# Optimization experiments

Measured on AMD Instinct MI355X. Metric: run time of the kernel, lower is better.

Reference implementation:

```python
import jax, jax.numpy as jnp
import numpy as np

B, L, D, H = 4, 2048, 1024, 16
DH = D // H
EPS = 1e-6

def layer_norm(x, g, b):
    mu = jnp.mean(x, axis=-1, keepdims=True)
    var = jnp.mean(jnp.square(x - mu), axis=-1, keepdims=True)
    return (x - mu) * jax.lax.rsqrt(var + EPS) * g + b

def setup_inputs() -> dict:
    key = jax.random.key(0)
    ks = jax.random.split(key, 8)
    s = 0.02
    return {
        "x": jax.random.normal(ks[0], (B, L, D), jnp.float32),
        "mask": jnp.ones((B, L), jnp.int32),
        "Wq": jax.random.normal(ks[1], (D, D), jnp.float32) * s,
        "bq": jnp.zeros((D,), jnp.float32),
        "Wk": jax.random.normal(ks[2], (D, D), jnp.float32) * s,
        "bk": jnp.zeros((D,), jnp.float32),
        "Wv": jax.random.normal(ks[3], (D, D), jnp.float32) * s,
        "bv": jnp.zeros((D,), jnp.float32),
        "g1": jnp.ones((D,), jnp.float32),
        "b1": jnp.zeros((D,), jnp.float32),
        "g2": jnp.ones((D,), jnp.float32),
        "b2": jnp.zeros((D,), jnp.float32),
        "Wo1": jax.random.normal(ks[4], (D, D), jnp.float32) * s,
        "bo1": jnp.zeros((D,), jnp.float32),
        "Wo2": jax.random.normal(ks[5], (D, D), jnp.float32) * s,
        "bo2": jnp.zeros((D,), jnp.float32),
    }

def reference(x, mask, Wq, bq, Wk, bk, Wv, bv, g1, b1, g2, b2, Wo1, bo1, Wo2, bo2):
    h = layer_norm(x, g1, b1)                                  # [B,L,D]
    q = (h @ Wq + bq).reshape(B, L, H, DH)
    k = (h @ Wk + bk).reshape(B, L, H, DH)
    v = (h @ Wv + bv).reshape(B, L, H, DH)
    scores = jnp.einsum('bqhd,bkhd->bhqk', q, k) / jnp.sqrt(jnp.float32(DH))
    m = mask.astype(scores.dtype)[:, None, None, :]            # [B,1,1,L]
    scores = scores + (1.0 - m) * (-1e30)                      # mask_logits
    probs = jax.nn.softmax(scores, axis=-1)
    attn = jnp.einsum('bhqk,bkhd->bqhd', probs, v).reshape(B, L, D)
    residual = x + attn
    out = layer_norm(residual, g2, b2)
    out = jax.nn.gelu(out @ Wo1 + bo1, approximate=False)      # exact GELU (nn.GELU)
    out = out @ Wo2 + bo2 + residual
    return out
```

## Files before the change

### kernel.cpp

```cpp
#include <hip/hip_runtime.h>
#include <stdint.h>
#include <math.h>

typedef __bf16 bf16_t;
typedef __bf16 bf16x8 __attribute__((ext_vector_type(8)));
typedef __bf16 bf16x4 __attribute__((ext_vector_type(4)));
typedef short short4v __attribute__((ext_vector_type(4)));
typedef float f32x4 __attribute__((ext_vector_type(4)));

#define B_ 4
#define L_ 2048
#define D_ 1024
#define H_ 16
#define DH_ 64
#define M_ (B_ * L_)
#define LOG2E 1.4426950408889634f
#define QSCALE 0.18033688011112042f

__device__ __forceinline__ void gload16(const bf16_t* gsrc, bf16_t* ldst) {
    __builtin_amdgcn_global_load_lds(
        (__attribute__((address_space(1))) void*)(void*)(gsrc),
        (__attribute__((address_space(3))) void*)(ldst), 16, 0, 0);
}

__device__ __forceinline__ float gelu_exact(float v) {
    return 0.5f * v * (1.0f + erff(v * 0.70710678118654752f));
}

__device__ __forceinline__ float fast_exp2(float x) {
#if __has_builtin(__builtin_amdgcn_exp2f)
    return __builtin_amdgcn_exp2f(x);
#else
    return exp2f(x);
#endif
}

__device__ __forceinline__ f32x4 mfma16(bf16x4 a, bf16x4 b, f32x4 c) {
#if __has_builtin(__builtin_amdgcn_mfma_f32_16x16x16_bf16)
    return __builtin_amdgcn_mfma_f32_16x16x16_bf16(a, b, c, 0, 0, 0);
#else
    union U { bf16x4 h; short4v s; };
    U ua, ub; ua.h = a; ub.h = b;
    return __builtin_amdgcn_mfma_f32_16x16x16bf16_1k(ua.s, ub.s, c, 0, 0, 0);
#endif
}

__global__ __launch_bounds__(256) void transpose5(const float* __restrict__ W0, const float* __restrict__ W1,
                                                  const float* __restrict__ W2, const float* __restrict__ W3,
                                                  const float* __restrict__ W4,
                                                  bf16_t* __restrict__ T0, bf16_t* __restrict__ T1,
                                                  bf16_t* __restrict__ T2, bf16_t* __restrict__ T3,
                                                  bf16_t* __restrict__ T4) {
    const float* W; bf16_t* T;
    switch (blockIdx.z) {
        case 0: W = W0; T = T0; break;
        case 1: W = W1; T = T1; break;
        case 2: W = W2; T = T2; break;
        case 3: W = W3; T = T3; break;
        default: W = W4; T = T4; break;
    }
    __shared__ float tile[32][33];
    const int x = threadIdx.x, y0 = threadIdx.y;
    const int bx = blockIdx.x * 32, by = blockIdx.y * 32;
    for (int kk = 0; kk < 4; ++kk)
        tile[y0 + kk * 8][x] = W[(size_t)(by + y0 + kk * 8) * D_ + bx + x];
    __syncthreads();
    for (int kk = 0; kk < 4; ++kk)
        T[(size_t)(bx + y0 + kk * 8) * D_ + by + x] = (bf16_t)tile[x][y0 + kk * 8];
}

__global__ __launch_bounds__(256) void maskbias_kernel(const int* __restrict__ mask,
                                                       float* __restrict__ mb) {
    const int i = blockIdx.x * 256 + threadIdx.x;
    mb[i] = mask[i] ? 0.f : -1.0e30f;
}

#define VTR_STRIDE 76
__global__ __launch_bounds__(256) void vtrans_kernel(const bf16_t* __restrict__ vb,
                                                     bf16_t* __restrict__ vt) {
    __shared__ bf16_t tile[128 * VTR_STRIDE];
    const int t = threadIdx.x;
    const int bh = blockIdx.y, b = bh >> 4, h = bh & 15;
    const int k0 = blockIdx.x * 128;
    #pragma unroll
    for (int it = 0; it < 4; ++it) {
        const int row = it * 32 + (t >> 3), c8 = (t & 7) * 8;
        *(uint4*)&tile[row * VTR_STRIDE + c8] =
            *(const uint4*)(vb + (size_t)(b * L_ + k0 + row) * D_ + h * DH_ + c8);
    }
    __syncthreads();
    #pragma unroll
    for (int it = 0; it < 4; ++it) {
        const int d = it * 16 + (t >> 4), kg = (t & 15) * 8;
        union { uint4 u; bf16_t e[8]; } tv;
        #pragma unroll
        for (int j = 0; j < 8; ++j) tv.e[j] = tile[(kg + j) * VTR_STRIDE + d];
        *(uint4*)&vt[((size_t)bh * DH_ + d) * L_ + k0 + kg] = tv.u;
    }
}

__global__ __launch_bounds__(256) void ln1_kernel(const float* __restrict__ x,
                                                  const float* __restrict__ g,
                                                  const float* __restrict__ b,
                                                  bf16_t* __restrict__ h) {
    const int row = blockIdx.x, t = threadIdx.x;
    const float4 v = *(const float4*)(x + (size_t)row * D_ + t * 4);
    float s = v.x + v.y + v.z + v.w;
    float s2 = v.x * v.x + v.y * v.y + v.z * v.z + v.w * v.w;
    for (int m = 1; m < 64; m <<= 1) { s += __shfl_xor(s, m, 64); s2 += __shfl_xor(s2, m, 64); }
    __shared__ float red[2][4];
    if ((t & 63) == 0) { red[0][t >> 6] = s; red[1][t >> 6] = s2; }
    __syncthreads();
    s = red[0][0] + red[0][1] + red[0][2] + red[0][3];
    s2 = red[1][0] + red[1][1] + red[1][2] + red[1][3];
    const float mean = s * (1.f / 1024.f);
    const float var = s2 * (1.f / 1024.f) - mean * mean;
    const float rstd = rsqrtf(var + 1e-6f);
    const float4 gv = *(const float4*)(g + t * 4);
    const float4 bv = *(const float4*)(b + t * 4);
    union { bf16_t h4[4]; uint2 u; } o;
    o.h4[0] = (bf16_t)((v.x - mean) * rstd * gv.x + bv.x);
    o.h4[1] = (bf16_t)((v.y - mean) * rstd * gv.y + bv.y);
    o.h4[2] = (bf16_t)((v.z - mean) * rstd * gv.z + bv.z);
    o.h4[3] = (bf16_t)((v.w - mean) * rstd * gv.w + bv.w);
    *(uint2*)(h + (size_t)row * D_ + t * 4) = o.u;
}

__global__ __launch_bounds__(256) void add_ln2_kernel(const float* __restrict__ x,
                                                      const bf16_t* __restrict__ attnb,
                                                      const float* __restrict__ g,
                                                      const float* __restrict__ b,
                                                      bf16_t* __restrict__ residb,
                                                      bf16_t* __restrict__ h) {
    const int row = blockIdx.x, t = threadIdx.x;
    const float4 xv = *(const float4*)(x + (size_t)row * D_ + t * 4);
    union { uint2 u; bf16_t h4[4]; } ai;
    ai.u = *(const uint2*)(attnb + (size_t)row * D_ + t * 4);
    float4 v;
    v.x = xv.x + (float)ai.h4[0]; v.y = xv.y + (float)ai.h4[1];
    v.z = xv.z + (float)ai.h4[2]; v.w = xv.w + (float)ai.h4[3];
    union { bf16_t h4[4]; uint2 u; } rs;
    rs.h4[0] = (bf16_t)v.x; rs.h4[1] = (bf16_t)v.y; rs.h4[2] = (bf16_t)v.z; rs.h4[3] = (bf16_t)v.w;
    *(uint2*)(residb + (size_t)row * D_ + t * 4) = rs.u;
    float s = v.x + v.y + v.z + v.w;
    float s2 = v.x * v.x + v.y * v.y + v.z * v.z + v.w * v.w;
    for (int m = 1; m < 64; m <<= 1) { s += __shfl_xor(s, m, 64); s2 += __shfl_xor(s2, m, 64); }
    __shared__ float red[2][4];
    if ((t & 63) == 0) { red[0][t >> 6] = s; red[1][t >> 6] = s2; }
    __syncthreads();
    s = red[0][0] + red[0][1] + red[0][2] + red[0][3];
    s2 = red[1][0] + red[1][1] + red[1][2] + red[1][3];
    const float mean = s * (1.f / 1024.f);
    const float var = s2 * (1.f / 1024.f) - mean * mean;
    const float rstd = rsqrtf(var + 1e-6f);
    const float4 gv = *(const float4*)(g + t * 4);
    const float4 bv = *(const float4*)(b + t * 4);
    union { bf16_t h4[4]; uint2 u; } o;
    o.h4[0] = (bf16_t)((v.x - mean) * rstd * gv.x + bv.x);
    o.h4[1] = (bf16_t)((v.y - mean) * rstd * gv.y + bv.y);
    o.h4[2] = (bf16_t)((v.z - mean) * rstd * gv.z + bv.z);
    o.h4[3] = (bf16_t)((v.w - mean) * rstd * gv.w + bv.w);
    *(uint2*)(h + (size_t)row * D_ + t * 4) = o.u;
}

__global__ __launch_bounds__(256) void gemm_qkv(const bf16_t* __restrict__ A,
                                                const bf16_t* __restrict__ BT,
                                                const float* __restrict__ bq,
                                                const float* __restrict__ bk,
                                                const float* __restrict__ bv,
                                                bf16_t* __restrict__ qb,
                                                bf16_t* __restrict__ kb,
                                                bf16_t* __restrict__ vb) {
    constexpr int K = 1024;
    __shared__ bf16_t As[128 * 32];
    __shared__ bf16_t Bs[128 * 32];
    const int t = threadIdx.x;
    const int wave = t >> 6, lane = t & 63;
    const int l16 = lane & 15, g4 = lane >> 4;
    const int bm = blockIdx.x * 128, bn = blockIdx.y * 128;
    const int wm = (wave >> 1) * 64, wn = (wave & 1) * 64;

    f32x4 acc[4][4];
    for (int i = 0; i < 4; ++i)
        for (int j = 0; j < 4; ++j) acc[i][j] = (f32x4){0.f, 0.f, 0.f, 0.f};

    const int ar = t >> 2, ak = (t & 3) * 8;
    const bf16_t* Ag = A + (size_t)(bm + ar) * K + ak;
    const bf16_t* Bg = BT + (size_t)(bn + ar) * K + ak;
    bf16_t* Al = As + t * 8;
    bf16_t* Bl = Bs + t * 8;

    for (int kk = 0; kk < K; kk += 32) {
        __syncthreads();
        gload16(Ag + kk, Al);
        gload16(Ag + (size_t)64 * K + kk, Al + 2048);
        gload16(Bg + kk, Bl);
        gload16(Bg + (size_t)64 * K + kk, Bl + 2048);
        __syncthreads();
        bf16x8 af[4], bfr[4];
        for (int i = 0; i < 4; ++i)
            af[i] = *(const bf16x8*)&As[(wm + i * 16 + l16) * 32 + g4 * 8];
        for (int j = 0; j < 4; ++j)
            bfr[j] = *(const bf16x8*)&Bs[(wn + j * 16 + l16) * 32 + g4 * 8];
        for (int i = 0; i < 4; ++i)
            for (int j = 0; j < 4; ++j)
                acc[i][j] = __builtin_amdgcn_mfma_f32_16x16x32_bf16(af[i], bfr[j], acc[i][j], 0, 0, 0);
    }

    const int which = bn >> 10;
    const int c0 = bn & 1023;
    const float* bias = (which == 0) ? bq : (which == 1) ? bk : bv;
    bf16_t* ob = (which == 0) ? qb : (which == 1) ? kb : vb;
    const float scale = (which == 0) ? QSCALE : 1.0f;

    for (int i = 0; i < 4; ++i)
        for (int j = 0; j < 4; ++j) {
            const int col = c0 + wn + j * 16 + l16;
            const float bvv = bias[col];
            const int row0 = bm + wm + i * 16 + g4 * 4;
            for (int r = 0; r < 4; ++r) {
                const float vv = (acc[i][j][r] + bvv) * scale;
                ob[(size_t)(row0 + r) * D_ + col] = (bf16_t)vv;
            }
        }
}

template <int MODE>
__global__ __launch_bounds__(256) void gemm_bt(const bf16_t* __restrict__ A,
                                               const bf16_t* __restrict__ BT,
                                               const float* __restrict__ bias,
                                               const bf16_t* __restrict__ residb,
                                               bf16_t* __restrict__ outb,
                                               float* __restrict__ outf) {
    constexpr int K = 1024, N = 1024;
    __shared__ bf16_t As[128 * 32];
    __shared__ bf16_t Bs[128 * 32];
    const int t = threadIdx.x;
    const int wave = t >> 6, lane = t & 63;
    const int l16 = lane & 15, g4 = lane >> 4;
    const int bm = blockIdx.x * 128, bn = blockIdx.y * 128;
    const int wm = (wave >> 1) * 64, wn = (wave & 1) * 64;

    f32x4 acc[4][4];
    for (int i = 0; i < 4; ++i)
        for (int j = 0; j < 4; ++j) acc[i][j] = (f32x4){0.f, 0.f, 0.f, 0.f};

    const int ar = t >> 2, ak = (t & 3) * 8;
    const bf16_t* Ag = A + (size_t)(bm + ar) * K + ak;
    const bf16_t* Bg = BT + (size_t)(bn + ar) * K + ak;
    bf16_t* Al = As + t * 8;
    bf16_t* Bl = Bs + t * 8;

    for (int kk = 0; kk < K; kk += 32) {
        __syncthreads();
        gload16(Ag + kk, Al);
        gload16(Ag + (size_t)64 * K + kk, Al + 2048);
        gload16(Bg + kk, Bl);
        gload16(Bg + (size_t)64 * K + kk, Bl + 2048);
        __syncthreads();
        bf16x8 af[4], bfr[4];
        for (int i = 0; i < 4; ++i)
            af[i] = *(const bf16x8*)&As[(wm + i * 16 + l16) * 32 + g4 * 8];
        for (int j = 0; j < 4; ++j)
            bfr[j] = *(const bf16x8*)&Bs[(wn + j * 16 + l16) * 32 + g4 * 8];
        for (int i = 0; i < 4; ++i)
            for (int j = 0; j < 4; ++j)
                acc[i][j] = __builtin_amdgcn_mfma_f32_16x16x32_bf16(af[i], bfr[j], acc[i][j], 0, 0, 0);
    }

    for (int i = 0; i < 4; ++i)
        for (int j = 0; j < 4; ++j) {
            const int col = bn + wn + j * 16 + l16;
            const float bv = bias[col];
            const int row0 = bm + wm + i * 16 + g4 * 4;
            for (int r = 0; r < 4; ++r) {
                float vv = acc[i][j][r] + bv;
                const size_t idx = (size_t)(row0 + r) * N + col;
                if (MODE == 1) {
                    outb[idx] = (bf16_t)gelu_exact(vv);
                } else {
                    outf[idx] = vv + (float)residb[idx];
                }
            }
        }
}

#define VT_STRIDE 152
#define OS_STRIDE 72
__global__ __launch_bounds__(256, 3) void attn_kernel(const bf16_t* __restrict__ q,
                                                      const bf16_t* __restrict__ k,
                                                      const bf16_t* __restrict__ vt,
                                                      const float* __restrict__ maskbias,
                                                      bf16_t* __restrict__ attnb) {
    __shared__ bf16_t Ks[128 * 64];
    __shared__ bf16_t VT[64 * VT_STRIDE];
    bf16_t* Os = VT;

    const int t = threadIdx.x;
    const int wave = t >> 6, lane = t & 63;
    const int l16 = lane & 15, g4 = lane >> 4;
    const int id = blockIdx.x;
    const int xcd = id & 7, seq = id >> 3;
    const int bh = xcd * 8 + (seq >> 4);
    const int b = bh >> 4, h = bh & 15;
    const int q0 = (seq & 15) * 128;

    bf16x8 qf[2][2];
    for (int ti = 0; ti < 2; ++ti)
        for (int c = 0; c < 2; ++c)
            qf[ti][c] = *(const bf16x8*)(q + (size_t)(b * L_ + q0 + wave * 32 + ti * 16 + l16) * D_ +
                                         h * DH_ + c * 32 + g4 * 8);

    f32x4 accO[2][5];
    for (int ti = 0; ti < 2; ++ti)
        for (int dt = 0; dt < 5; ++dt) accO[ti][dt] = (f32x4){0.f, 0.f, 0.f, 0.f};

    const bf16_t one_or_zero = (l16 == 0) ? (bf16_t)1.0f : (bf16_t)0.0f;
    const bf16x4 ones4 = (bf16x4){one_or_zero, one_or_zero, one_or_zero, one_or_zero};

    const int krow0 = t >> 3, kcg = t & 7;
    const int klcg = kcg ^ (krow0 & 7);
    const bf16_t* kbase = k + (size_t)(b * L_ + krow0) * D_ + h * DH_ + klcg * 8;
    bf16_t* kdst = Ks + t * 8;
    const int vrow0 = t >> 4, vkg = t & 15;
    const bf16_t* vbase = vt + ((size_t)bh * DH_ + vrow0) * L_ + vkg * 8;
    bf16_t* vdst = &VT[vrow0 * VT_STRIDE + vkg * 8];

    const int kb0 = l16 * 64 + ((g4 ^ (l16 & 7)) * 8);
    const int kb1 = l16 * 64 + (((g4 + 4) ^ (l16 & 7)) * 8);
    const int vrb = l16 * VT_STRIDE + g4 * 4;

    for (int k0 = 0; k0 < L_; k0 += 128) {
        __syncthreads();
        #pragma unroll
        for (int it = 0; it < 4; ++it)
            gload16(kbase + (size_t)(k0 + it * 32) * D_, kdst + it * 2048);
        #pragma unroll
        for (int it = 0; it < 4; ++it) {
            const uint4 vv = *(const uint4*)(vbase + (size_t)(it * 16) * L_ + k0);
            *(uint4*)(vdst + it * 16 * VT_STRIDE) = vv;
        }
        __syncthreads();

        f32x4 s0[8], s1[8];
        #pragma unroll
        for (int tj = 0; tj < 8; ++tj) {
            const bf16x8 kf0 = *(const bf16x8*)&Ks[tj * 1024 + kb0];
            const bf16x8 kf1 = *(const bf16x8*)&Ks[tj * 1024 + kb1];
            f32x4 a = (f32x4){0.f, 0.f, 0.f, 0.f};
            a = __builtin_amdgcn_mfma_f32_16x16x32_bf16(kf0, qf[0][0], a, 0, 0, 0);
            a = __builtin_amdgcn_mfma_f32_16x16x32_bf16(kf1, qf[0][1], a, 0, 0, 0);
            s0[tj] = a;
            f32x4 a2 = (f32x4){0.f, 0.f, 0.f, 0.f};
            a2 = __builtin_amdgcn_mfma_f32_16x16x32_bf16(kf0, qf[1][0], a2, 0, 0, 0);
            a2 = __builtin_amdgcn_mfma_f32_16x16x32_bf16(kf1, qf[1][1], a2, 0, 0, 0);
            s1[tj] = a2;
        }

        bf16x4 pb0[8], pb1[8];
        #pragma unroll
        for (int tj = 0; tj < 8; ++tj) {
            const float4 mb = *(const float4*)&maskbias[b * L_ + k0 + tj * 16 + g4 * 4];
            float p00 = fast_exp2(s0[tj][0] + mb.x), p01 = fast_exp2(s0[tj][1] + mb.y);
            float p02 = fast_exp2(s0[tj][2] + mb.z), p03 = fast_exp2(s0[tj][3] + mb.w);
            float p10 = fast_exp2(s1[tj][0] + mb.x), p11 = fast_exp2(s1[tj][1] + mb.y);
            float p12 = fast_exp2(s1[tj][2] + mb.z), p13 = fast_exp2(s1[tj][3] + mb.w);
            pb0[tj] = (bf16x4){(bf16_t)p00, (bf16_t)p01, (bf16_t)p02, (bf16_t)p03};
            pb1[tj] = (bf16x4){(bf16_t)p10, (bf16_t)p11, (bf16_t)p12, (bf16_t)p13};
        }

        #pragma unroll
        for (int ks = 0; ks < 8; ++ks) {
            #pragma unroll
            for (int dt = 0; dt < 4; ++dt) {
                const bf16x4 va = *(const bf16x4*)&VT[vrb + dt * 16 * VT_STRIDE + ks * 16];
                accO[0][dt] = mfma16(va, pb0[ks], accO[0][dt]);
                accO[1][dt] = mfma16(va, pb1[ks], accO[1][dt]);
            }
            accO[0][4] = mfma16(ones4, pb0[ks], accO[0][4]);
            accO[1][4] = mfma16(ones4, pb1[ks], accO[1][4]);
        }
    }

    __syncthreads();
    for (int ti = 0; ti < 2; ++ti) {
        const float lv = __shfl(accO[ti][4][0], l16, 64);
        const float rl = 1.0f / lv;
        #pragma unroll
        for (int dt = 0; dt < 4; ++dt) {
            bf16x4 o4 = (bf16x4){(bf16_t)(accO[ti][dt][0] * rl), (bf16_t)(accO[ti][dt][1] * rl),
                                 (bf16_t)(accO[ti][dt][2] * rl), (bf16_t)(accO[ti][dt][3] * rl)};
            *(bf16x4*)&Os[(wave * 32 + ti * 16 + l16) * OS_STRIDE + dt * 16 + g4 * 4] = o4;
        }
    }
    __syncthreads();
    for (int cc = 0; cc < 4; ++cc) {
        const int c2 = t + cc * 256;
        const int row = c2 >> 3, k8 = c2 & 7;
        const uint4 vv = *(const uint4*)&Os[row * OS_STRIDE + k8 * 8];
        *(uint4*)&attnb[(size_t)(b * L_ + q0 + row) * D_ + h * DH_ + k8 * 8] = vv;
    }
}

extern "C" void kernel_launch(void* const* d_in, const int* in_sizes, int n_in,
                              void* d_out, int out_size, void* d_ws, size_t ws_size,
                              hipStream_t stream) {
    const float* x    = (const float*)d_in[0];
    const int*   mask = (const int*)d_in[1];
    const float* Wq   = (const float*)d_in[2];
    const float* bq   = (const float*)d_in[3];
    const float* Wk   = (const float*)d_in[4];
    const float* bk   = (const float*)d_in[5];
    const float* Wv   = (const float*)d_in[6];
    const float* bv   = (const float*)d_in[7];
    const float* g1   = (const float*)d_in[8];
    const float* b1   = (const float*)d_in[9];
    const float* g2   = (const float*)d_in[10];
    const float* b2   = (const float*)d_in[11];
    const float* Wo1  = (const float*)d_in[12];
    const float* bo1  = (const float*)d_in[13];
    const float* Wo2  = (const float*)d_in[14];
    const float* bo2  = (const float*)d_in[15];

    char* ws = (char*)d_ws;
    const size_t MBs = 1ull << 20;
    bf16_t* WqkvT = (bf16_t*)(ws + 0 * MBs);
    bf16_t* Wo1T  = (bf16_t*)(ws + 6 * MBs);
    bf16_t* Wo2T  = (bf16_t*)(ws + 8 * MBs);
    bf16_t* h1    = (bf16_t*)(ws + 10 * MBs);
    bf16_t* vtb   = h1;
    bf16_t* qb    = (bf16_t*)(ws + 26 * MBs);
    bf16_t* kb    = (bf16_t*)(ws + 42 * MBs);
    bf16_t* vb    = (bf16_t*)(ws + 58 * MBs);
    bf16_t* attnb = (bf16_t*)(ws + 74 * MBs);
    bf16_t* residb= (bf16_t*)(ws + 90 * MBs);
    float*  mbias = (float*)(ws + 106 * MBs);
    bf16_t* h2    = qb;
    bf16_t* gact  = kb;

    transpose5<<<dim3(32, 32, 5), dim3(32, 8), 0, stream>>>(
        Wq, Wk, Wv, Wo1, Wo2,
        WqkvT, WqkvT + (size_t)D_ * D_, WqkvT + (size_t)2 * D_ * D_, Wo1T, Wo2T);

    maskbias_kernel<<<M_ / 256, 256, 0, stream>>>(mask, mbias);

    ln1_kernel<<<M_, 256, 0, stream>>>(x, g1, b1, h1);

    gemm_qkv<<<dim3(M_ / 128, 3 * D_ / 128), 256, 0, stream>>>(h1, WqkvT, bq, bk, bv, qb, kb, vb);

    vtrans_kernel<<<dim3(L_ / 128, B_ * H_), 256, 0, stream>>>(vb, vtb);

    attn_kernel<<<dim3(1024), 256, 0, stream>>>(qb, kb, vtb, mbias, attnb);

    add_ln2_kernel<<<M_, 256, 0, stream>>>(x, attnb, g2, b2, residb, h2);

    const dim3 gg(M_ / 128, D_ / 128);
    gemm_bt<1><<<gg, 256, 0, stream>>>(h2, Wo1T, bo1, nullptr, gact, nullptr);
    gemm_bt<2><<<gg, 256, 0, stream>>>(gact, Wo2T, bo2, residb, nullptr, (float*)d_out);
}
```

Measured before the change: 374.9 us.

## Skip mask-bias loads for fully-unmasked key tiles and use 16x16x32 MFMA for PV

```diff
diff --git a/kernel.cpp b/kernel.cpp
--- a/kernel.cpp
+++ b/kernel.cpp
@@ -5,7 +5,6 @@
 typedef __bf16 bf16_t;
 typedef __bf16 bf16x8 __attribute__((ext_vector_type(8)));
 typedef __bf16 bf16x4 __attribute__((ext_vector_type(4)));
-typedef short short4v __attribute__((ext_vector_type(4)));
 typedef float f32x4 __attribute__((ext_vector_type(4)));
 
 #define B_ 4
@@ -14,7 +13,6 @@
 #define H_ 16
 #define DH_ 64
 #define M_ (B_ * L_)
-#define LOG2E 1.4426950408889634f
 #define QSCALE 0.18033688011112042f
 
 __device__ __forceinline__ void gload16(const bf16_t* gsrc, bf16_t* ldst) {
@@ -32,16 +30,6 @@
     return __builtin_amdgcn_exp2f(x);
 #else
     return exp2f(x);
-#endif
-}
-
-__device__ __forceinline__ f32x4 mfma16(bf16x4 a, bf16x4 b, f32x4 c) {
-#if __has_builtin(__builtin_amdgcn_mfma_f32_16x16x16_bf16)
-    return __builtin_amdgcn_mfma_f32_16x16x16_bf16(a, b, c, 0, 0, 0);
-#else
-    union U { bf16x4 h; short4v s; };
-    U ua, ub; ua.h = a; ub.h = b;
-    return __builtin_amdgcn_mfma_f32_16x16x16bf16_1k(ua.s, ub.s, c, 0, 0, 0);
 #endif
 }
 
@@ -70,9 +58,18 @@
 }
 
 __global__ __launch_bounds__(256) void maskbias_kernel(const int* __restrict__ mask,
-                                                       float* __restrict__ mb) {
+                                                       float* __restrict__ mb,
+                                                       unsigned char* __restrict__ flags) {
     const int i = blockIdx.x * 256 + threadIdx.x;
-    mb[i] = mask[i] ? 0.f : -1.0e30f;
+    const int m = mask[i];
+    mb[i] = m ? 0.f : -1.0e30f;
+    const unsigned long long bal = __ballot(m != 0);
+    __shared__ unsigned char ok[4];
+    if ((threadIdx.x & 63) == 0) ok[threadIdx.x >> 6] = (bal == ~0ull) ? 1 : 0;
+    __syncthreads();
+    if (threadIdx.x < 2)
+        flags[blockIdx.x * 2 + threadIdx.x] =
+            (unsigned char)(ok[threadIdx.x * 2] & ok[threadIdx.x * 2 + 1]);
 }
 
 #define VTR_STRIDE 76
@@ -91,11 +88,15 @@
     __syncthreads();
     #pragma unroll
     for (int it = 0; it < 4; ++it) {
-        const int d = it * 16 + (t >> 4), kg = (t & 15) * 8;
+        const int d = it * 16 + (t >> 4), pos0 = (t & 15) * 8;
+        const int base32 = pos0 & ~31, g = (pos0 >> 3) & 3;
         union { uint4 u; bf16_t e[8]; } tv;
         #pragma unroll
-        for (int j = 0; j < 8; ++j) tv.e[j] = tile[(kg + j) * VTR_STRIDE + d];
-        *(uint4*)&vt[((size_t)bh * DH_ + d) * L_ + k0 + kg] = tv.u;
+        for (int j = 0; j < 8; ++j) {
+            const int kk = base32 + ((j >> 2) << 4) + (g << 2) + (j & 3);
+            tv.e[j] = tile[kk * VTR_STRIDE + d];
+        }
+        *(uint4*)&vt[((size_t)bh * DH_ + d) * L_ + k0 + pos0] = tv.u;
     }
 }
 
@@ -291,6 +292,7 @@
                                                       const bf16_t* __restrict__ k,
                                                       const bf16_t* __restrict__ vt,
                                                       const float* __restrict__ maskbias,
+                                                      const unsigned char* __restrict__ mflags,
                                                       bf16_t* __restrict__ attnb) {
     __shared__ bf16_t Ks[128 * 64];
     __shared__ bf16_t VT[64 * VT_STRIDE];
@@ -315,8 +317,8 @@
     for (int ti = 0; ti < 2; ++ti)
         for (int dt = 0; dt < 5; ++dt) accO[ti][dt] = (f32x4){0.f, 0.f, 0.f, 0.f};
 
-    const bf16_t one_or_zero = (l16 == 0) ? (bf16_t)1.0f : (bf16_t)0.0f;
-    const bf16x4 ones4 = (bf16x4){one_or_zero, one_or_zero, one_or_zero, one_or_zero};
+    const bf16_t ozv = (l16 == 0) ? (bf16_t)1.0f : (bf16_t)0.0f;
+    const bf16x8 ones8 = (bf16x8){ozv, ozv, ozv, ozv, ozv, ozv, ozv, ozv};
 
     const int krow0 = t >> 3, kcg = t & 7;
     const int klcg = kcg ^ (krow0 & 7);
@@ -328,7 +330,8 @@
 
     const int kb0 = l16 * 64 + ((g4 ^ (l16 & 7)) * 8);
     const int kb1 = l16 * 64 + (((g4 + 4) ^ (l16 & 7)) * 8);
-    const int vrb = l16 * VT_STRIDE + g4 * 4;
+    const int vrb = l16 * VT_STRIDE + g4 * 8;
+    const unsigned char* flg = mflags + b * 16;
 
     for (int k0 = 0; k0 < L_; k0 += 128) {
         __syncthreads();
@@ -357,28 +360,38 @@
             s1[tj] = a2;
         }
 
-        bf16x4 pb0[8], pb1[8];
-        #pragma unroll
-        for (int tj = 0; tj < 8; ++tj) {
-            const float4 mb = *(const float4*)&maskbias[b * L_ + k0 + tj * 16 + g4 * 4];
-            float p00 = fast_exp2(s0[tj][0] + mb.x), p01 = fast_exp2(s0[tj][1] + mb.y);
-            float p02 = fast_exp2(s0[tj][2] + mb.z), p03 = fast_exp2(s0[tj][3] + mb.w);
-            float p10 = fast_exp2(s1[tj][0] + mb.x), p11 = fast_exp2(s1[tj][1] + mb.y);
-            float p12 = fast_exp2(s1[tj][2] + mb.z), p13 = fast_exp2(s1[tj][3] + mb.w);
-            pb0[tj] = (bf16x4){(bf16_t)p00, (bf16_t)p01, (bf16_t)p02, (bf16_t)p03};
-            pb1[tj] = (bf16x4){(bf16_t)p10, (bf16_t)p11, (bf16_t)p12, (bf16_t)p13};
-        }
-
-        #pragma unroll
-        for (int ks = 0; ks < 8; ++ks) {
+        if (!flg[k0 >> 7]) {
+            #pragma unroll
+            for (int tj = 0; tj < 8; ++tj) {
+                const float4 mb = *(const float4*)&maskbias[b * L_ + k0 + tj * 16 + g4 * 4];
+                s0[tj][0] += mb.x; s0[tj][1] += mb.y; s0[tj][2] += mb.z; s0[tj][3] += mb.w;
+                s1[tj][0] += mb.x; s1[tj][1] += mb.y; s1[tj][2] += mb.z; s1[tj][3] += mb.w;
+            }
+        }
+
+        bf16x8 pb0[4], pb1[4];
+        #pragma unroll
+        for (int c = 0; c < 4; ++c) {
+            pb0[c] = (bf16x8){(bf16_t)fast_exp2(s0[2 * c][0]), (bf16_t)fast_exp2(s0[2 * c][1]),
+                              (bf16_t)fast_exp2(s0[2 * c][2]), (bf16_t)fast_exp2(s0[2 * c][3]),
+                              (bf16_t)fast_exp2(s0[2 * c + 1][0]), (bf16_t)fast_exp2(s0[2 * c + 1][1]),
+                              (bf16_t)fast_exp2(s0[2 * c + 1][2]), (bf16_t)fast_exp2(s0[2 * c + 1][3])};
+            pb1[c] = (bf16x8){(bf16_t)fast_exp2(s1[2 * c][0]), (bf16_t)fast_exp2(s1[2 * c][1]),
+                              (bf16_t)fast_exp2(s1[2 * c][2]), (bf16_t)fast_exp2(s1[2 * c][3]),
+                              (bf16_t)fast_exp2(s1[2 * c + 1][0]), (bf16_t)fast_exp2(s1[2 * c + 1][1]),
+                              (bf16_t)fast_exp2(s1[2 * c + 1][2]), (bf16_t)fast_exp2(s1[2 * c + 1][3])};
+        }
+
+        #pragma unroll
+        for (int c = 0; c < 4; ++c) {
             #pragma unroll
             for (int dt = 0; dt < 4; ++dt) {
-                const bf16x4 va = *(const bf16x4*)&VT[vrb + dt * 16 * VT_STRIDE + ks * 16];
-                accO[0][dt] = mfma16(va, pb0[ks], accO[0][dt]);
-                accO[1][dt] = mfma16(va, pb1[ks], accO[1][dt]);
+                const bf16x8 va = *(const bf16x8*)&VT[vrb + dt * 16 * VT_STRIDE + c * 32];
+                accO[0][dt] = __builtin_amdgcn_mfma_f32_16x16x32_bf16(va, pb0[c], accO[0][dt], 0, 0, 0);
+                accO[1][dt] = __builtin_amdgcn_mfma_f32_16x16x32_bf16(va, pb1[c], accO[1][dt], 0, 0, 0);
             }
-            accO[0][4] = mfma16(ones4, pb0[ks], accO[0][4]);
-            accO[1][4] = mfma16(ones4, pb1[ks], accO[1][4]);
+            accO[0][4] = __builtin_amdgcn_mfma_f32_16x16x32_bf16(ones8, pb0[c], accO[0][4], 0, 0, 0);
+            accO[1][4] = __builtin_amdgcn_mfma_f32_16x16x32_bf16(ones8, pb1[c], accO[1][4], 0, 0, 0);
         }
     }
 
@@ -435,6 +448,7 @@
     bf16_t* attnb = (bf16_t*)(ws + 74 * MBs);
     bf16_t* residb= (bf16_t*)(ws + 90 * MBs);
     float*  mbias = (float*)(ws + 106 * MBs);
+    unsigned char* mflags = (unsigned char*)(ws + 107 * MBs);
     bf16_t* h2    = qb;
     bf16_t* gact  = kb;
 
@@ -442,7 +456,7 @@
         Wq, Wk, Wv, Wo1, Wo2,
         WqkvT, WqkvT + (size_t)D_ * D_, WqkvT + (size_t)2 * D_ * D_, Wo1T, Wo2T);
 
-    maskbias_kernel<<<M_ / 256, 256, 0, stream>>>(mask, mbias);
+    maskbias_kernel<<<M_ / 256, 256, 0, stream>>>(mask, mbias, mflags);
 
     ln1_kernel<<<M_, 256, 0, stream>>>(x, g1, b1, h1);
 
@@ -450,7 +464,7 @@
 
     vtrans_kernel<<<dim3(L_ / 128, B_ * H_), 256, 0, stream>>>(vb, vtb);
 
-    attn_kernel<<<dim3(1024), 256, 0, stream>>>(qb, kb, vtb, mbias, attnb);
+    attn_kernel<<<dim3(1024), 256, 0, stream>>>(qb, kb, vtb, mbias, mflags, attnb);
 
     add_ln2_kernel<<<M_, 256, 0, stream>>>(x, attnb, g2, b2, residb, h2);
 
```

Result: faster. 341.1 us (-9.0%).
